# Kernel optimization log

Measured on AMD Instinct MI355X. Metric: run time of the kernel, lower is better.

Reference implementation:

```python
import jax, jax.numpy as jnp
import numpy as np

N, IN_DIM, E_DIM, H, D = 10000, 128, 32, 4, 32
NE = 640000
OUT_DIM = D  # out Linear maps H*D -> out_dim == D here (32)


def setup_inputs() -> dict:
    key = jax.random.key(0)
    ks = jax.random.split(key, 12)
    HD = H * D
    s = lambda k, sh, fan: jax.random.normal(k, sh, jnp.float32) / np.sqrt(fan)
    return {
        "x": jax.random.normal(ks[0], (N, IN_DIM), jnp.float32),
        "edge_index": jax.random.randint(ks[1], (2, NE), 0, N),
        "edge_attr": jax.random.normal(ks[2], (NE, E_DIM), jnp.float32),
        "Wq": s(ks[3], (IN_DIM, HD), IN_DIM), "bq": jnp.zeros((HD,), jnp.float32),
        "Wk": s(ks[4], (IN_DIM, HD), IN_DIM), "bk": jnp.zeros((HD,), jnp.float32),
        "Wv": s(ks[5], (IN_DIM, HD), IN_DIM), "bv": jnp.zeros((HD,), jnp.float32),
        "We": s(ks[6], (E_DIM, HD), E_DIM), "be": jnp.zeros((HD,), jnp.float32),
        "Wo": s(ks[7], (HD, OUT_DIM), HD), "bo": jnp.zeros((OUT_DIM,), jnp.float32),
    }


def reference(x, edge_index, edge_attr, Wq, bq, Wk, bk, Wv, bv, We, be, Wo, bo):
    n = x.shape[0]
    Q = (x @ Wq + bq).reshape(-1, H, D)
    K = (x @ Wk + bk).reshape(-1, H, D)
    V = (x @ Wv + bv).reshape(-1, H, D)
    Ef = (edge_attr @ We + be).reshape(-1, H, D)
    src, dst = edge_index[0], edge_index[1]
    # per-edge scores [E, H]: QK dot over src/dst gather + E self dot
    scores = (jnp.einsum('ehd,ehd->eh', Q[src], K[dst])
              + jnp.einsum('ehd,ehd->eh', Ef, Ef)) / np.sqrt(D).astype(np.float32)
    alpha = jax.nn.softmax(scores, axis=-1)  # softmax over heads (as in source)
    out_e = (alpha[..., None] * V[dst]).reshape(-1, H * D)  # [E, H*D]
    out_e = out_e @ Wo + bo  # [E, out_dim]
    # scatter-mean by source node
    sums = jax.ops.segment_sum(out_e, src, num_segments=n)
    cnt = jax.ops.segment_sum(jnp.ones((out_e.shape[0],), out_e.dtype), src, num_segments=n)
    return sums / jnp.maximum(cnt, 1.0)[:, None]
```

## Files before the change

kernel.cpp:

```cpp
#include <hip/hip_runtime.h>

#define NN      10000
#define IN_DIM  128
#define E_DIM   32
#define NH      4
#define DH      32
#define HD      128
#define NE_     640000
#define OUT_DIM 32
#define SCAN_T  1024
#define CHUNK   10
#define NTILES  (NN / 16)
#define NTASKS  (NTILES * 3)
#define QKVP_BLKS  469
#define EE_BLKS    (NE_ / 256)
#define HIST_BLKS  (NE_ / 256)

typedef __attribute__((ext_vector_type(8))) short bf16x8;
typedef __attribute__((ext_vector_type(4))) float f32x4;

static __device__ __forceinline__ unsigned short f32_to_bf16_rne(float f) {
    unsigned u = __float_as_uint(f);
    return (unsigned short)((u + 0x7fffu + ((u >> 16) & 1u)) >> 16);
}
static __device__ __forceinline__ float bf16_bits_to_f32(unsigned short h) {
    return __uint_as_float(((unsigned)h) << 16);
}
static __device__ __forceinline__ float blo(unsigned u) { return __uint_as_float(u << 16); }
static __device__ __forceinline__ float bhi(unsigned u) { return __uint_as_float(u & 0xffff0000u); }

__global__ __launch_bounds__(256) void prep_kernel(
    const float* __restrict__ Wq, const float* __restrict__ Wk,
    const float* __restrict__ Wv, const float* __restrict__ Wo,
    const float* __restrict__ bv, const float* __restrict__ We,
    const int*   __restrict__ ei,
    unsigned short* __restrict__ wfh, unsigned short* __restrict__ wfl,
    unsigned short* __restrict__ wefh, unsigned short* __restrict__ wefl,
    float* __restrict__ bp,
    int* __restrict__ deg, int* __restrict__ rank)
{
    const int blk = blockIdx.x;
    const int t = threadIdx.x;

    if (blk < 24) {
        const int tid = blk * 256 + t;
        const int l = tid & 63;
        const int ts = tid >> 6;
        const int s = ts & 3, tt = ts >> 2;
        const int col = (tt & 7) * 16 + (l & 15);
        if (tt < 16) {
            const float* __restrict__ W = (tt < 8) ? Wq : Wk;
            #pragma unroll
            for (int j = 0; j < 8; ++j) {
                const int k = s * 32 + (l >> 4) * 8 + j;
                const float w = W[k * HD + col];
                const unsigned short hi = f32_to_bf16_rne(w);
                wfh[tid * 8 + j] = hi;
                wfl[tid * 8 + j] = f32_to_bf16_rne(w - bf16_bits_to_f32(hi));
            }
        } else {
            const int h = col & 3, oo = col >> 2;
            #pragma unroll
            for (int j = 0; j < 8; ++j) {
                const int k = s * 32 + (l >> 4) * 8 + j;
                float acc = 0.f;
                #pragma unroll
                for (int d2 = 0; d2 < DH; ++d2)
                    acc = fmaf(Wv[k * HD + h * DH + d2],
                               Wo[(h * DH + d2) * OUT_DIM + oo], acc);
                const unsigned short hi = f32_to_bf16_rne(acc);
                wfh[tid * 8 + j] = hi;
                wfl[tid * 8 + j] = f32_to_bf16_rne(acc - bf16_bits_to_f32(hi));
            }
        }
    } else if (blk < 26) {
        const int tid = (blk - 24) * 256 + t;
        const int l = tid & 63, tt = tid >> 6;
        #pragma unroll
        for (int j = 0; j < 8; ++j) {
            const int k = (l >> 4) * 8 + j;
            const int d = tt * 16 + (l & 15);
            const float w = We[k * HD + d];
            const unsigned short hi = f32_to_bf16_rne(w);
            wefh[tid * 8 + j] = hi;
            wefl[tid * 8 + j] = f32_to_bf16_rne(w - bf16_bits_to_f32(hi));
        }
    } else if (blk == 26) {
        if (t < HD) {
            const int h = t & 3, oo = t >> 2;
            float b = 0.f;
            #pragma unroll
            for (int d2 = 0; d2 < DH; ++d2)
                b = fmaf(bv[h * DH + d2], Wo[(h * DH + d2) * OUT_DIM + oo], b);
            bp[t] = b;
        }
    } else {
        const int e = (blk - 27) * 256 + t;
        rank[e] = atomicAdd(&deg[ei[e]], 1);
    }
}

__global__ __launch_bounds__(SCAN_T) void scan_kernel(
    const int* __restrict__ deg, int* __restrict__ off)
{
    __shared__ int wsum[16];
    const int t = threadIdx.x;
    const int lane = t & 63, w = t >> 6;
    const int base = t * CHUNK;
    int v[CHUNK];
    int sum = 0;
    #pragma unroll
    for (int i = 0; i < CHUNK; ++i) {
        const int idx = base + i;
        v[i] = (idx < NN) ? deg[idx] : 0;
        sum += v[i];
    }
    int incl = sum;
    #pragma unroll
    for (int dlt = 1; dlt < 64; dlt <<= 1) {
        const int nb = __shfl_up(incl, dlt, 64);
        if (lane >= dlt) incl += nb;
    }
    if (lane == 63) wsum[w] = incl;
    __syncthreads();
    if (w == 0) {
        const int val = (lane < 16) ? wsum[lane] : 0;
        int wi = val;
        #pragma unroll
        for (int dlt = 1; dlt < 16; dlt <<= 1) {
            const int nb = __shfl_up(wi, dlt, 64);
            if (lane >= dlt) wi += nb;
        }
        if (lane < 16) wsum[lane] = wi - val;
    }
    __syncthreads();
    int run = wsum[w] + (incl - sum);
    #pragma unroll
    for (int i = 0; i < CHUNK; ++i) {
        const int idx = base + i;
        if (idx < NN) { off[idx] = run; run += v[i]; }
    }
}

__global__ __launch_bounds__(256) void mm_kernel(
    const float* __restrict__ x,
    const unsigned short* __restrict__ wfh, const unsigned short* __restrict__ wfl,
    const float* __restrict__ bq, const float* __restrict__ bk,
    const float* __restrict__ bp,
    float* __restrict__ Q, unsigned short* __restrict__ KPTb,
    const float* __restrict__ ea,
    const unsigned short* __restrict__ wefh, const unsigned short* __restrict__ wefl,
    const float* __restrict__ be,
    const int* __restrict__ ei,
    const int* __restrict__ off, const int* __restrict__ rank,
    float4* __restrict__ pay)
{
    const int lane = threadIdx.x & 63;
    const int wave = threadIdx.x >> 6;

    if (blockIdx.x < QKVP_BLKS) {
        const int task = blockIdx.x * 4 + wave;
        if (task >= NTASKS) return;
        const int nt = task / 3, cg = task - nt * 3;
        const int node = nt * 16 + (lane & 15);
        const int kc = lane >> 4;

        bf16x8 xh0, xl0, xh1, xl1, xh2, xl2, xh3, xl3;
#define SPL(VH, VL, I, VAL) { \
    const unsigned short hh = f32_to_bf16_rne(VAL); \
    VH[I] = (short)hh; VL[I] = (short)f32_to_bf16_rne((VAL) - bf16_bits_to_f32(hh)); }
#define LOAD_X(S, VH, VL) { \
    const float* xr = x + (size_t)node * IN_DIM + (S) * 32 + kc * 8; \
    const float4 a0 = *reinterpret_cast<const float4*>(xr); \
    const float4 a1 = *reinterpret_cast<const float4*>(xr + 4); \
    SPL(VH, VL, 0, a0.x) SPL(VH, VL, 1, a0.y) SPL(VH, VL, 2, a0.z) SPL(VH, VL, 3, a0.w) \
    SPL(VH, VL, 4, a1.x) SPL(VH, VL, 5, a1.y) SPL(VH, VL, 6, a1.z) SPL(VH, VL, 7, a1.w) }
        LOAD_X(0, xh0, xl0) LOAD_X(1, xh1, xl1) LOAD_X(2, xh2, xl2) LOAD_X(3, xh3, xl3)
#undef LOAD_X
#undef SPL

        const float* __restrict__ bb = (cg == 0) ? bq : (cg == 1) ? bk : bp;

#define KSTEP(S, FB, FB2, XH, XL) { \
    const bf16x8 wh = *reinterpret_cast<const bf16x8*>((FB)  + (S) * 64 * 8); \
    const bf16x8 wl = *reinterpret_cast<const bf16x8*>((FB2) + (S) * 64 * 8); \
    acc = __builtin_amdgcn_mfma_f32_16x16x32_bf16(wh, XH, acc, 0, 0, 0); \
    acc = __builtin_amdgcn_mfma_f32_16x16x32_bf16(wh, XL, acc, 0, 0, 0); \
    acc = __builtin_amdgcn_mfma_f32_16x16x32_bf16(wl, XH, acc, 0, 0, 0); }

#define TILE(TLOC) { \
    const unsigned short* fb  = wfh + ((((cg * 8 + TLOC) * 4) * 64 + lane) << 3); \
    const unsigned short* fb2 = wfl + ((((cg * 8 + TLOC) * 4) * 64 + lane) << 3); \
    const float4 b4 = *reinterpret_cast<const float4*>(bb + (TLOC) * 16 + (kc << 2)); \
    f32x4 acc = {b4.x, b4.y, b4.z, b4.w}; \
    KSTEP(0, fb, fb2, xh0, xl0) KSTEP(1, fb, fb2, xh1, xl1) \
    KSTEP(2, fb, fb2, xh2, xl2) KSTEP(3, fb, fb2, xh3, xl3) \
    const int j0 = (TLOC) * 16 + (kc << 2); \
    if (cg == 0) { \
        *reinterpret_cast<float4*>(Q + (size_t)node * HD + j0) = \
            make_float4(acc[0], acc[1], acc[2], acc[3]); \
    } else { \
        unsigned short* dp = KPTb + (size_t)node * 256 + j0 * 2 + ((cg == 1) ? 0 : 4); \
        *reinterpret_cast<ushort4*>(dp) = make_ushort4( \
            f32_to_bf16_rne(acc[0]), f32_to_bf16_rne(acc[1]), \
            f32_to_bf16_rne(acc[2]), f32_to_bf16_rne(acc[3])); \
    } }

        TILE(0) TILE(1) TILE(2) TILE(3) TILE(4) TILE(5) TILE(6) TILE(7)
#undef TILE
#undef KSTEP
        return;
    }

    const int base = (blockIdx.x - QKVP_BLKS) * 256 + wave * 64;

    const int src  = ei[base + lane];
    const int dstn = ei[NE_ + base + lane];
    const int pos  = off[src] + rank[base + lane];

    const int erow = lane & 15;
    const int kc = lane >> 4;
    bf16x8 ah0, ah1, ah2, ah3;
#define LOAD_A(AT, VAR) { \
    const float* ar = ea + (size_t)(base + AT * 16 + erow) * E_DIM + kc * 8; \
    const float4 a0 = *reinterpret_cast<const float4*>(ar); \
    const float4 a1 = *reinterpret_cast<const float4*>(ar + 4); \
    VAR[0] = (short)f32_to_bf16_rne(a0.x); VAR[1] = (short)f32_to_bf16_rne(a0.y); \
    VAR[2] = (short)f32_to_bf16_rne(a0.z); VAR[3] = (short)f32_to_bf16_rne(a0.w); \
    VAR[4] = (short)f32_to_bf16_rne(a1.x); VAR[5] = (short)f32_to_bf16_rne(a1.y); \
    VAR[6] = (short)f32_to_bf16_rne(a1.z); VAR[7] = (short)f32_to_bf16_rne(a1.w); }
    LOAD_A(0, ah0) LOAD_A(1, ah1) LOAD_A(2, ah2) LOAD_A(3, ah3)
#undef LOAD_A

    float p00 = 0.f, p01 = 0.f, p02 = 0.f, p03 = 0.f;
    float p10 = 0.f, p11 = 0.f, p12 = 0.f, p13 = 0.f;
    float p20 = 0.f, p21 = 0.f, p22 = 0.f, p23 = 0.f;
    float p30 = 0.f, p31 = 0.f, p32 = 0.f, p33 = 0.f;

#define AT_BODY(AT, H, WHI, WLO, BE4) { \
    f32x4 acc = {BE4.x, BE4.y, BE4.z, BE4.w}; \
    acc = __builtin_amdgcn_mfma_f32_16x16x32_bf16(WLO, ah##AT, acc, 0, 0, 0); \
    acc = __builtin_amdgcn_mfma_f32_16x16x32_bf16(WHI, ah##AT, acc, 0, 0, 0); \
    p##AT##H = fmaf(acc[0], acc[0], fmaf(acc[1], acc[1], \
               fmaf(acc[2], acc[2], fmaf(acc[3], acc[3], p##AT##H)))); }

#define TILE(T, H) { \
    const bf16x8 whi = *reinterpret_cast<const bf16x8*>(wefh + ((T * 64 + lane) << 3)); \
    const bf16x8 wlo = *reinterpret_cast<const bf16x8*>(wefl + ((T * 64 + lane) << 3)); \
    const float4 be4 = *reinterpret_cast<const float4*>(be + T * 16 + ((lane >> 4) << 2)); \
    AT_BODY(0, H, whi, wlo, be4) AT_BODY(1, H, whi, wlo, be4) \
    AT_BODY(2, H, whi, wlo, be4) AT_BODY(3, H, whi, wlo, be4) }

    TILE(0, 0) TILE(1, 0) TILE(2, 1) TILE(3, 1)
    TILE(4, 2) TILE(5, 2) TILE(6, 3) TILE(7, 3)
#undef TILE
#undef AT_BODY

#define RED(AT, H) \
    float r##AT##H = p##AT##H; \
    r##AT##H += __shfl_xor(r##AT##H, 16, 64); \
    r##AT##H += __shfl_xor(r##AT##H, 32, 64);
    RED(0, 0) RED(0, 1) RED(0, 2) RED(0, 3)
    RED(1, 0) RED(1, 1) RED(1, 2) RED(1, 3)
    RED(2, 0) RED(2, 1) RED(2, 2) RED(2, 3)
    RED(3, 0) RED(3, 1) RED(3, 2) RED(3, 3)
#undef RED

    const int at4 = lane >> 4;
#define SEL(H) ((at4 & 2) ? ((at4 & 1) ? r3##H : r2##H) : ((at4 & 1) ? r1##H : r0##H))
    const float w0 = SEL(0), w1 = SEL(1), w2 = SEL(2), w3 = SEL(3);
#undef SEL

    pay[pos] = make_float4(__int_as_float(dstn), w0 - w3, w1 - w3, w2 - w3);
}

__global__ __launch_bounds__(256) void fused_gather_kernel(
    const int* __restrict__ off, const int* __restrict__ deg,
    const float4* __restrict__ pay,
    const float* __restrict__ Q, const unsigned short* __restrict__ KPTb,
    const float* __restrict__ bo, float* __restrict__ out)
{
    __shared__ float red[16][OUT_DIM];
    const int n = blockIdx.x;
    const int d = deg[n];
    const int start = off[n];
    const int tid = threadIdx.x;
    const int g = tid >> 4;
    const int o16 = tid & 15;
    const int h = o16 >> 2;
    const float scale = 0.17677669529663687f;

    const float* __restrict__ qrow = Q + (size_t)n * HD + o16 * 8;
    const float4 qa = *reinterpret_cast<const float4*>(qrow);
    const float4 qb = *reinterpret_cast<const float4*>(qrow + 4);

    float acc0 = 0.f, acc1 = 0.f;

    float4 pc = make_float4(0.f, 0.f, 0.f, 0.f);
    float4 pn = make_float4(0.f, 0.f, 0.f, 0.f);
    if (g < d)      pc = pay[start + g];
    if (g + 16 < d) pn = pay[start + g + 16];
    uint4 uc0, uc1;
    {
        const unsigned short* __restrict__ kp =
            KPTb + (size_t)__float_as_int(pc.x) * 256 + o16 * 16;
        uc0 = *reinterpret_cast<const uint4*>(kp);
        uc1 = *reinterpret_cast<const uint4*>(kp + 8);
    }

    for (int i = g; i < d; i += 16) {
        float4 pn2 = make_float4(0.f, 0.f, 0.f, 0.f);
        if (i + 32 < d) pn2 = pay[start + i + 32];
        uint4 un0 = make_uint4(0, 0, 0, 0), un1 = make_uint4(0, 0, 0, 0);
        if (i + 16 < d) {
            const unsigned short* __restrict__ kp =
                KPTb + (size_t)__float_as_int(pn.x) * 256 + o16 * 16;
            un0 = *reinterpret_cast<const uint4*>(kp);
            un1 = *reinterpret_cast<const uint4*>(kp + 8);
        }

        float p =           qa.x * blo(uc0.x);
        p = fmaf(qa.y, bhi(uc0.x), p);
        p = fmaf(qa.z, blo(uc0.y), p);
        p = fmaf(qa.w, bhi(uc0.y), p);
        p = fmaf(qb.x, blo(uc1.x), p);
        p = fmaf(qb.y, bhi(uc1.x), p);
        p = fmaf(qb.z, blo(uc1.y), p);
        p = fmaf(qb.w, bhi(uc1.y), p);
        p += __shfl_xor(p, 1, 64);
        p += __shfl_xor(p, 2, 64);
        const float b  = __shfl_xor(p, 4, 64);
        const float e0 = (h & 1) ? b : p;
        const float e1 = (h & 1) ? p : b;
        const float o0 = __shfl_xor(e0, 8, 64);
        const float o1 = __shfl_xor(e1, 8, 64);
        const float qk0 = (h & 2) ? o0 : e0;
        const float qk1 = (h & 2) ? o1 : e1;
        const float qk2 = (h & 2) ? e0 : o0;
        const float qk3 = (h & 2) ? e1 : o1;

        const float s0 = (qk0 + pc.y) * scale;
        const float s1 = (qk1 + pc.z) * scale;
        const float s2 = (qk2 + pc.w) * scale;
        const float s3 = qk3 * scale;
        const float mx = fmaxf(fmaxf(s0, s1), fmaxf(s2, s3));
        const float a0 = __expf(s0 - mx), a1 = __expf(s1 - mx);
        const float a2 = __expf(s2 - mx), a3 = __expf(s3 - mx);
        const float inv = 1.f / (a0 + a1 + a2 + a3);

        float c0 =          a0 * blo(uc0.z);
        c0 = fmaf(a1, bhi(uc0.z), c0);
        c0 = fmaf(a2, blo(uc0.w), c0);
        c0 = fmaf(a3, bhi(uc0.w), c0);
        float c1 =          a0 * blo(uc1.z);
        c1 = fmaf(a1, bhi(uc1.z), c1);
        c1 = fmaf(a2, blo(uc1.w), c1);
        c1 = fmaf(a3, bhi(uc1.w), c1);
        acc0 = fmaf(c0, inv, acc0);
        acc1 = fmaf(c1, inv, acc1);

        pc = pn; pn = pn2; uc0 = un0; uc1 = un1;
    }
    red[g][o16 * 2]     = acc0;
    red[g][o16 * 2 + 1] = acc1;
    __syncthreads();
    if (tid < 32) {
        float s = 0.f;
        #pragma unroll
        for (int gg = 0; gg < 16; ++gg) s += red[gg][tid];
        out[(size_t)n * OUT_DIM + tid] = (d > 0) ? (s / (float)d + bo[tid]) : 0.f;
    }
}

extern "C" void kernel_launch(void* const* d_in, const int* in_sizes, int n_in,
                              void* d_out, int out_size, void* d_ws, size_t ws_size,
                              hipStream_t stream)
{
    const float* x   = (const float*)d_in[0];
    const int*   ei  = (const int*)  d_in[1];
    const float* ea  = (const float*)d_in[2];
    const float* Wq  = (const float*)d_in[3];
    const float* bq  = (const float*)d_in[4];
    const float* Wk  = (const float*)d_in[5];
    const float* bk  = (const float*)d_in[6];
    const float* Wv  = (const float*)d_in[7];
    const float* bv  = (const float*)d_in[8];
    const float* We  = (const float*)d_in[9];
    const float* be  = (const float*)d_in[10];
    const float* Wo  = (const float*)d_in[11];
    const float* bo  = (const float*)d_in[12];
    float* out = (float*)d_out;

    float*  Q    = (float*)d_ws;
    float4* pay  = (float4*)(Q + (size_t)NN * HD);
    unsigned short* KPTb = (unsigned short*)(pay + NE_);
    float*  bp   = (float*)(KPTb + (size_t)NN * 256);
    unsigned short* wefh = (unsigned short*)(bp + HD);
    unsigned short* wefl = wefh + 8 * 64 * 8;
    unsigned short* wfh  = wefl + 8 * 64 * 8;
    unsigned short* wfl  = wfh + 24 * 4 * 64 * 8;
    int* rank = (int*)(wfl + 24 * 4 * 64 * 8);
    int* deg  = rank + NE_;
    int* off  = deg + NN;

    hipMemsetAsync(deg, 0, NN * sizeof(int), stream);

    prep_kernel<<<27 + HIST_BLKS, 256, 0, stream>>>(Wq, Wk, Wv, Wo, bv, We, ei,
                                                    wfh, wfl, wefh, wefl, bp,
                                                    deg, rank);
    scan_kernel<<<1, SCAN_T, 0, stream>>>(deg, off);
    mm_kernel<<<QKVP_BLKS + EE_BLKS, 256, 0, stream>>>(x, wfh, wfl, bq, bk, bp,
                                                       Q, KPTb, ea, wefh, wefl,
                                                       be, ei, off, rank, pay);
    fused_gather_kernel<<<NN, 256, 0, stream>>>(off, deg, pay, Q, KPTb, bo, out);
}
```

Measured before the change: 124.6 us.

## Map one wave per node in gather kernel and reorder mm_kernel block roles

The gather kernel now gives each node a single 64-lane wave instead of a 256-thread block. With four nodes per block, the LDS reduction and __syncthreads are replaced by cross-lane shuffles, and the edge loop strides by 4 instead of 16. The aim is to avoid idle threads on low-degree nodes (average degree is about 64) and to cut block launch and sync overhead. In exchange, each wave runs a longer serial chain of edges per node. Separately, mm_kernel now schedules the edge blocks before the QKV projection blocks, which changes their dispatch order.

```diff
diff --git a/kernel.cpp b/kernel.cpp
--- a/kernel.cpp
+++ b/kernel.cpp
@@ -158,8 +158,8 @@
     const int lane = threadIdx.x & 63;
     const int wave = threadIdx.x >> 6;
 
-    if (blockIdx.x < QKVP_BLKS) {
-        const int task = blockIdx.x * 4 + wave;
+    if (blockIdx.x >= EE_BLKS) {
+        const int task = (blockIdx.x - EE_BLKS) * 4 + wave;
         if (task >= NTASKS) return;
         const int nt = task / 3, cg = task - nt * 3;
         const int node = nt * 16 + (lane & 15);
@@ -212,7 +212,7 @@
         return;
     }
 
-    const int base = (blockIdx.x - QKVP_BLKS) * 256 + wave * 64;
+    const int base = blockIdx.x * 256 + wave * 64;
 
     const int src  = ei[base + lane];
     const int dstn = ei[NE_ + base + lane];
@@ -280,13 +280,15 @@
     const float* __restrict__ Q, const unsigned short* __restrict__ KPTb,
     const float* __restrict__ bo, float* __restrict__ out)
 {
-    __shared__ float red[16][OUT_DIM];
-    const int n = blockIdx.x;
+    const int lane = threadIdx.x & 63;
+    const int wave = threadIdx.x >> 6;
+    const int n = blockIdx.x * 4 + wave;
+    if (n >= NN) return;
+
     const int d = deg[n];
     const int start = off[n];
-    const int tid = threadIdx.x;
-    const int g = tid >> 4;
-    const int o16 = tid & 15;
+    const int g = lane >> 4;
+    const int o16 = lane & 15;
     const int h = o16 >> 2;
     const float scale = 0.17677669529663687f;
 
@@ -298,8 +300,8 @@
 
     float4 pc = make_float4(0.f, 0.f, 0.f, 0.f);
     float4 pn = make_float4(0.f, 0.f, 0.f, 0.f);
-    if (g < d)      pc = pay[start + g];
-    if (g + 16 < d) pn = pay[start + g + 16];
+    if (g < d)     pc = pay[start + g];
+    if (g + 4 < d) pn = pay[start + g + 4];
     uint4 uc0, uc1;
     {
         const unsigned short* __restrict__ kp =
@@ -308,11 +310,11 @@
         uc1 = *reinterpret_cast<const uint4*>(kp + 8);
     }
 
-    for (int i = g; i < d; i += 16) {
+    for (int i = g; i < d; i += 4) {
         float4 pn2 = make_float4(0.f, 0.f, 0.f, 0.f);
-        if (i + 32 < d) pn2 = pay[start + i + 32];
+        if (i + 8 < d) pn2 = pay[start + i + 8];
         uint4 un0 = make_uint4(0, 0, 0, 0), un1 = make_uint4(0, 0, 0, 0);
-        if (i + 16 < d) {
+        if (i + 4 < d) {
             const unsigned short* __restrict__ kp =
                 KPTb + (size_t)__float_as_int(pn.x) * 256 + o16 * 16;
             un0 = *reinterpret_cast<const uint4*>(kp);
@@ -361,14 +363,17 @@
 
         pc = pn; pn = pn2; uc0 = un0; uc1 = un1;
     }
-    red[g][o16 * 2]     = acc0;
-    red[g][o16 * 2 + 1] = acc1;
-    __syncthreads();
-    if (tid < 32) {
-        float s = 0.f;
-        #pragma unroll
-        for (int gg = 0; gg < 16; ++gg) s += red[gg][tid];
-        out[(size_t)n * OUT_DIM + tid] = (d > 0) ? (s / (float)d + bo[tid]) : 0.f;
+
+    acc0 += __shfl_xor(acc0, 16, 64);
+    acc0 += __shfl_xor(acc0, 32, 64);
+    acc1 += __shfl_xor(acc1, 16, 64);
+    acc1 += __shfl_xor(acc1, 32, 64);
+    if (lane < 16) {
+        const float2 b2 = *reinterpret_cast<const float2*>(bo + o16 * 2);
+        float2 r;
+        r.x = (d > 0) ? (acc0 / (float)d + b2.x) : 0.f;
+        r.y = (d > 0) ? (acc1 / (float)d + b2.y) : 0.f;
+        *reinterpret_cast<float2*>(out + (size_t)n * OUT_DIM + o16 * 2) = r;
     }
 }
 
@@ -409,8 +414,9 @@
                                                     wfh, wfl, wefh, wefl, bp,
                                                     deg, rank);
     scan_kernel<<<1, SCAN_T, 0, stream>>>(deg, off);
-    mm_kernel<<<QKVP_BLKS + EE_BLKS, 256, 0, stream>>>(x, wfh, wfl, bq, bk, bp,
+    mm_kernel<<<EE_BLKS + QKVP_BLKS, 256, 0, stream>>>(x, wfh, wfl, bq, bk, bp,
                                                        Q, KPTb, ea, wefh, wefl,
                                                        be, ei, off, rank, pay);
-    fused_gather_kernel<<<NN, 256, 0, stream>>>(off, deg, pay, Q, KPTb, bo, out);
-}
+    fused_gather_kernel<<<(NN + 3) / 4, 256, 0, stream>>>(off, deg, pay, Q, KPTb,
+                                                          bo, out);
+}
```

Result: slower. 132.9 us (+6.6%).
